# Optimization experiments

Measured on AMD Instinct MI355X. Metric: run time of the kernel, lower is better.

## Reference

```python
import jax, jax.numpy as jnp
import numpy as np

BS, NA = 32, 128
NE = NA * (NA - 1)            # fully-connected directed, no self loops
NU, D = 4, 8                  # num_user, per-user feature dim
FEAT = NU * D                 # 32: node / edge feature dim
CC = 8                        # conv1 out channels (1x1 conv, in_channels=2)
CONV_OUT = CC * NU * D        # 256
EMB = 64                      # embedding size (x_last / output dim)
H1 = 256                      # MLP hidden
MLP1_IN = CONV_OUT + EMB      # layer_idx > 1: concat local_state_j
MLP2_IN = FEAT + EMB + EMB    # x0, x_last, agg_in


def make_edges():
    src, dst = np.meshgrid(np.arange(NA), np.arange(NA), indexing='ij')
    m = src != dst
    return jnp.asarray(np.stack([src[m], dst[m]], axis=1), dtype=jnp.int32)


def setup_inputs() -> dict:
    key = jax.random.key(0)
    ks = jax.random.split(key, 9)
    return {
        "x0": jax.random.normal(ks[0], (BS, NA, FEAT), jnp.float32),
        "x_last": jax.random.normal(ks[1], (BS, NA, EMB), jnp.float32),
        "edge_attr": jax.random.normal(ks[2], (BS, NE, FEAT), jnp.float32),
        "conv_w": jax.random.normal(ks[3], (CC, 2), jnp.float32) * 0.3,
        "conv_b": jnp.zeros((CC,), jnp.float32),
        "mlp1_w1": jax.random.normal(ks[4], (MLP1_IN, H1), jnp.float32) * 0.05,
        "mlp1_b1": jnp.zeros((H1,), jnp.float32),
        "mlp1_w2": jax.random.normal(ks[5], (H1, EMB), jnp.float32) * 0.05,
        "mlp1_b2": jnp.zeros((EMB,), jnp.float32),
        "mlp2_w1": jax.random.normal(ks[6], (MLP2_IN, H1), jnp.float32) * 0.05,
        "mlp2_b1": jnp.zeros((H1,), jnp.float32),
        "mlp2_w2": jax.random.normal(ks[7], (H1, EMB), jnp.float32) * 0.05,
        "mlp2_b2": jnp.zeros((EMB,), jnp.float32),
        "edge_idx": make_edges(),
    }


def reference(x0, x_last, edge_attr, conv_w, conv_b,
              mlp1_w1, mlp1_b1, mlp1_w2, mlp1_b2,
              mlp2_w1, mlp2_b1, mlp2_w2, mlp2_b2, edge_idx):
    src, dst = edge_idx[:, 0], edge_idx[:, 1]
    # --- propagate / local_embedding ---
    nf_j = x0[:, src, :]                 # [B, E, FEAT] gather source node feats
    ls_j = x_last[:, src, :]             # [B, E, EMB]  (layer_idx > 1)
    # torch: cat(node_feat, edge_attr) on user dim then view [N,2,NU,D]
    x = jnp.stack([nf_j.reshape(BS, NE, NU, D),
                   edge_attr.reshape(BS, NE, NU, D)], axis=2)  # [B,E,2,NU,D]
    # 1x1 Conv2d(2 -> CC) + ReLU
    y = jax.nn.relu(jnp.einsum('becud,oc->beoud', x, conv_w)
                    + conv_b[None, None, :, None, None])
    y = y.reshape(BS, NE, CONV_OUT)
    lf = jnp.concatenate([y, ls_j], axis=-1)                   # [B,E,MLP1_IN]
    h = jax.nn.relu(lf @ mlp1_w1 + mlp1_b1)
    local_embed = h @ mlp1_w2 + mlp1_b2                        # [B,E,EMB]
    # per-node segment sum over destination (replaces python loop over agents)
    agg_in = jnp.zeros((BS, NA, EMB), local_embed.dtype).at[:, dst, :].add(local_embed)
    # --- update_embedding ---
    agg = jnp.concatenate([x0, x_last, agg_in], axis=-1)       # [B,NA,MLP2_IN]
    h2 = jax.nn.relu(agg @ mlp2_w1 + mlp2_b1)
    return h2 @ mlp2_w2 + mlp2_b2                              # [B,NA,EMB]
```

## Files before the change

### kernel.cpp

```cpp
#include <hip/hip_runtime.h>
#include <hip/hip_bf16.h>

#define BSg   32
#define NAg   128
#define NEg   16256
#define EMBg  64
#define H1g   256

typedef __attribute__((ext_vector_type(8))) short  short8;
typedef __attribute__((ext_vector_type(4))) float  f32x4;

__device__ __forceinline__ unsigned short f2bf16u(float x) {
    union { __hip_bfloat16 h; unsigned short u; } cv;
    cv.h = __float2bfloat16(x);
    return cv.u;
}
__device__ __forceinline__ unsigned int pack2(float a, float b) {
    union { __hip_bfloat162 h; unsigned int u; } cv;
    cv.h = __float22bfloat162_rn(make_float2(a, b));
    return cv.u;
}

__global__ void pack_weights(const float* __restrict__ w1, const float* __restrict__ xl,
                             unsigned short* __restrict__ w1p, unsigned short* __restrict__ xlp)
{
    int i = blockIdx.x * 256 + threadIdx.x;
    if (i < 320 * 256) {
        int k = i >> 8, n = i & 255;
        w1p[(k >> 3) * (256 * 8) + n * 8 + (k & 7)] = f2bf16u(w1[i]);
    }
    if (i < BSg * NAg * EMBg)
        xlp[i] = f2bf16u(xl[i]);
}

__global__ __launch_bounds__(512, 4) void edge_kernel(
    const float* __restrict__ x0, const unsigned short* __restrict__ xlp,
    const float* __restrict__ edge_attr, const float* __restrict__ conv_w,
    const float* __restrict__ conv_b, const unsigned short* __restrict__ w1p,
    const float* __restrict__ b1, const float* __restrict__ w2f,
    const float* __restrict__ b2, float* __restrict__ agg)
{
    __shared__ unsigned short fragA[2][8 * 4 * 64 * 8];

    const int tid  = threadIdx.x;
    const int b    = blockIdx.x >> 7;
    const int d    = blockIdx.x & 127;
    const int w8   = tid >> 6, lane = tid & 63;
    const int half = w8 >> 2, wq = w8 & 3;
    const int llo  = lane & 15, lhi = lane >> 4;
    const int colbase = wq * 64;

    short8 af8[4], af9[4];
    #pragma unroll
    for (int m = 0; m < 4; ++m) {
        int el = half * 64 + m * 16 + llo;
        int s  = el + (el >= d ? 1 : 0);
        if (s > 127) s = 127;
        const unsigned short* base = xlp + (((b << 7) | s) << 6) + lhi * 8;
        af8[m] = *(const short8*)base;
        af9[m] = *(const short8*)(base + 32);
    }

    {
        const int j  = wq * 16 + llo;
        const int el = half * 64 + j;
        int s = el + (el >= d ? 1 : 0);
        if (s > 127) s = 127;
        int e = s * 127 + d - (s < d ? 1 : 0);
        if (e > NEg - 1) e = NEg - 1;

        const float4* nfp = (const float4*)(x0        + (((size_t)b * NAg + s) << 5) + (lhi << 3));
        const float4* eap = (const float4*)(edge_attr + (((size_t)b * NEg + e) << 5) + (lhi << 3));
        float4 nf0 = nfp[0], nf1 = nfp[1];
        float4 ea0 = eap[0], ea1 = eap[1];

        #pragma unroll
        for (int o = 0; o < 8; ++o) {
            const float w0 = conv_w[2 * o], w1v = conv_w[2 * o + 1], cb = conv_b[o];
            float y0 = fmaxf(fmaf(w0, nf0.x, fmaf(w1v, ea0.x, cb)), 0.f);
            float y1 = fmaxf(fmaf(w0, nf0.y, fmaf(w1v, ea0.y, cb)), 0.f);
            float y2 = fmaxf(fmaf(w0, nf0.z, fmaf(w1v, ea0.z, cb)), 0.f);
            float y3 = fmaxf(fmaf(w0, nf0.w, fmaf(w1v, ea0.w, cb)), 0.f);
            float y4 = fmaxf(fmaf(w0, nf1.x, fmaf(w1v, ea1.x, cb)), 0.f);
            float y5 = fmaxf(fmaf(w0, nf1.y, fmaf(w1v, ea1.y, cb)), 0.f);
            float y6 = fmaxf(fmaf(w0, nf1.z, fmaf(w1v, ea1.z, cb)), 0.f);
            float y7 = fmaxf(fmaf(w0, nf1.w, fmaf(w1v, ea1.w, cb)), 0.f);
            uint4 pk;
            pk.x = pack2(y0, y1); pk.y = pack2(y2, y3);
            pk.z = pack2(y4, y5); pk.w = pack2(y6, y7);
            *(uint4*)&fragA[half][(((o * 4 + wq) * 64) + lane) * 8] = pk;
        }
    }
    __syncthreads();

    f32x4 acc[4][4];
    #pragma unroll
    for (int m = 0; m < 4; ++m)
        #pragma unroll
        for (int n = 0; n < 4; ++n)
            acc[m][n] = (f32x4){0.f, 0.f, 0.f, 0.f};

    #pragma unroll
    for (int ks = 0; ks < 10; ++ks) {
        short8 af[4], bf[4];
        #pragma unroll
        for (int m = 0; m < 4; ++m) {
            if (ks < 8)       af[m] = *(const short8*)&fragA[half][((ks * 4 + m) * 64 + lane) * 8];
            else if (ks == 8) af[m] = af8[m];
            else              af[m] = af9[m];
        }
        #pragma unroll
        for (int n = 0; n < 4; ++n)
            bf[n] = *(const short8*)&w1p[((ks * 4 + lhi) * H1g + colbase + n * 16 + llo) * 8];
        #pragma unroll
        for (int m = 0; m < 4; ++m)
            #pragma unroll
            for (int n = 0; n < 4; ++n)
                acc[m][n] = __builtin_amdgcn_mfma_f32_16x16x32_bf16(af[m], bf[n], acc[m][n], 0, 0, 0);
    }

    float h1s[4];
    {
        float bias1[4];
        #pragma unroll
        for (int n = 0; n < 4; ++n) bias1[n] = b1[colbase + n * 16 + llo];
        #pragma unroll
        for (int n = 0; n < 4; ++n) {
            float p = 0.f;
            #pragma unroll
            for (int m = 0; m < 4; ++m)
                #pragma unroll
                for (int i = 0; i < 4; ++i) {
                    float v = fmaxf(acc[m][n][i] + bias1[n], 0.f);
                    if (!(m == 3 && i == 3) || !(half == 1 && lhi == 3)) p += v;
                }
            p += __shfl_xor(p, 16, 64);
            p += __shfl_xor(p, 32, 64);
            h1s[n] = p;
        }
    }
    __syncthreads();

    float* h1part = (float*)&fragA[0][0];
    float* redS   = h1part + 512;

    if (lhi == 0) {
        #pragma unroll
        for (int n = 0; n < 4; ++n) h1part[half * 256 + colbase + n * 16 + llo] = h1s[n];
    }
    __syncthreads();

    {
        const int c = tid & 63, kq = tid >> 6;
        float p = 0.f;
        #pragma unroll 8
        for (int k0 = 0; k0 < 32; ++k0) {
            int k = kq * 32 + k0;
            float h = h1part[k] + h1part[256 + k];
            p = fmaf(h, w2f[k * 64 + c], p);
        }
        redS[kq * 64 + c] = p;
    }
    __syncthreads();
    if (tid < 64) {
        float v = redS[tid]       + redS[64 + tid]  + redS[128 + tid] + redS[192 + tid]
                + redS[256 + tid] + redS[320 + tid] + redS[384 + tid] + redS[448 + tid]
                + 127.f * b2[tid];
        agg[(((size_t)b * NAg + d) << 6) + tid] = v;
    }
}

__global__ __launch_bounds__(256) void node_kernel(
    const float* __restrict__ x0, const float* __restrict__ x_last,
    const float* __restrict__ agg, const float* __restrict__ w1,
    const float* __restrict__ b1, const float* __restrict__ w2,
    const float* __restrict__ b2, float* __restrict__ out)
{
    __shared__ float lf[8][160];
    __shared__ float h2s[8][257];
    const int tid = threadIdx.x;
    const int r0  = blockIdx.x * 8;

    for (int idx = tid; idx < 8 * 160; idx += 256) {
        int r = idx / 160, c = idx % 160;
        int gr = r0 + r;
        int bb = gr >> 7, a = gr & 127;
        float v;
        if (c < 32)      v = x0[(((size_t)bb * NAg + a) << 5) + c];
        else if (c < 96) v = x_last[(((size_t)bb * NAg + a) << 6) + (c - 32)];
        else             v = agg[((size_t)gr << 6) + (c - 96)];
        lf[r][c] = v;
    }
    __syncthreads();

    {
        const int c = tid;
        float acc[8];
        const float bb = b1[c];
        #pragma unroll
        for (int r = 0; r < 8; ++r) acc[r] = bb;
        for (int k = 0; k < 160; ++k) {
            float wv = w1[k * 256 + c];
            #pragma unroll
            for (int r = 0; r < 8; ++r) acc[r] = fmaf(lf[r][k], wv, acc[r]);
        }
        #pragma unroll
        for (int r = 0; r < 8; ++r) h2s[r][c] = fmaxf(acc[r], 0.f);
    }
    __syncthreads();

    {
        const int n = tid & 63, rq = tid >> 6;
        float acc[2];
        const float bb = b2[n];
        #pragma unroll
        for (int j = 0; j < 2; ++j) acc[j] = bb;
        for (int k = 0; k < 256; ++k) {
            float wv = w2[k * 64 + n];
            #pragma unroll
            for (int j = 0; j < 2; ++j) acc[j] = fmaf(h2s[rq * 2 + j][k], wv, acc[j]);
        }
        #pragma unroll
        for (int j = 0; j < 2; ++j)
            out[((size_t)(r0 + rq * 2 + j) << 6) + n] = acc[j];
    }
}

extern "C" void kernel_launch(void* const* d_in, const int* in_sizes, int n_in,
                              void* d_out, int out_size, void* d_ws, size_t ws_size,
                              hipStream_t stream)
{
    const float* x0       = (const float*)d_in[0];
    const float* x_last   = (const float*)d_in[1];
    const float* edge_attr= (const float*)d_in[2];
    const float* conv_w   = (const float*)d_in[3];
    const float* conv_b   = (const float*)d_in[4];
    const float* mlp1_w1  = (const float*)d_in[5];
    const float* mlp1_b1  = (const float*)d_in[6];
    const float* mlp1_w2  = (const float*)d_in[7];
    const float* mlp1_b2  = (const float*)d_in[8];
    const float* mlp2_w1  = (const float*)d_in[9];
    const float* mlp2_b1  = (const float*)d_in[10];
    const float* mlp2_w2  = (const float*)d_in[11];
    const float* mlp2_b2  = (const float*)d_in[12];

    char* ws = (char*)d_ws;
    float* agg          = (float*)ws;
    unsigned short* w1p = (unsigned short*)(ws + (1 << 20));
    unsigned short* xlp = (unsigned short*)(ws + (1 << 20) + (192 << 10));

    pack_weights<<<1024, 256, 0, stream>>>(mlp1_w1, x_last, w1p, xlp);
    edge_kernel<<<BSg * NAg, 512, 0, stream>>>(x0, xlp, edge_attr, conv_w, conv_b,
                                               w1p, mlp1_b1, mlp1_w2, mlp1_b2, agg);
    node_kernel<<<(BSg * NAg) / 8, 256, 0, stream>>>(x0, x_last, agg, mlp2_w1, mlp2_b1,
                                                     mlp2_w2, mlp2_b2, (float*)d_out);
}
```

Measured before the change: 141.1 us.

## Split edge kernel into half-blocks and move second MLP layer to separate kernel

```diff
diff --git a/kernel.cpp b/kernel.cpp
--- a/kernel.cpp
+++ b/kernel.cpp
@@ -33,20 +33,21 @@
         xlp[i] = f2bf16u(xl[i]);
 }
 
-__global__ __launch_bounds__(512, 4) void edge_kernel(
+__global__ __launch_bounds__(256, 5) void edge_kernel(
     const float* __restrict__ x0, const unsigned short* __restrict__ xlp,
     const float* __restrict__ edge_attr, const float* __restrict__ conv_w,
     const float* __restrict__ conv_b, const unsigned short* __restrict__ w1p,
-    const float* __restrict__ b1, const float* __restrict__ w2f,
-    const float* __restrict__ b2, float* __restrict__ agg)
-{
-    __shared__ unsigned short fragA[2][8 * 4 * 64 * 8];
+    const float* __restrict__ b1, float* __restrict__ h1half)
+{
+    __shared__ unsigned short fragA[8 * 4 * 64 * 8];
+
+    const int wgid = (blockIdx.x & 7) * 1024 + (blockIdx.x >> 3);
+    const int half = wgid & 1;
+    const int bd   = wgid >> 1;
+    const int b    = bd >> 7, d = bd & 127;
 
     const int tid  = threadIdx.x;
-    const int b    = blockIdx.x >> 7;
-    const int d    = blockIdx.x & 127;
-    const int w8   = tid >> 6, lane = tid & 63;
-    const int half = w8 >> 2, wq = w8 & 3;
+    const int wq   = tid >> 6, lane = tid & 63;
     const int llo  = lane & 15, lhi = lane >> 4;
     const int colbase = wq * 64;
 
@@ -88,7 +89,7 @@
             uint4 pk;
             pk.x = pack2(y0, y1); pk.y = pack2(y2, y3);
             pk.z = pack2(y4, y5); pk.w = pack2(y6, y7);
-            *(uint4*)&fragA[half][(((o * 4 + wq) * 64) + lane) * 8] = pk;
+            *(uint4*)&fragA[(((o * 4 + wq) * 64) + lane) * 8] = pk;
         }
     }
     __syncthreads();
@@ -105,7 +106,7 @@
         short8 af[4], bf[4];
         #pragma unroll
         for (int m = 0; m < 4; ++m) {
-            if (ks < 8)       af[m] = *(const short8*)&fragA[half][((ks * 4 + m) * 64 + lane) * 8];
+            if (ks < 8)       af[m] = *(const short8*)&fragA[((ks * 4 + m) * 64 + lane) * 8];
             else if (ks == 8) af[m] = af8[m];
             else              af[m] = af9[m];
         }
@@ -139,35 +140,26 @@
             h1s[n] = p;
         }
     }
-    __syncthreads();
-
-    float* h1part = (float*)&fragA[0][0];
-    float* redS   = h1part + 512;
 
     if (lhi == 0) {
         #pragma unroll
-        for (int n = 0; n < 4; ++n) h1part[half * 256 + colbase + n * 16 + llo] = h1s[n];
-    }
-    __syncthreads();
-
-    {
-        const int c = tid & 63, kq = tid >> 6;
-        float p = 0.f;
-        #pragma unroll 8
-        for (int k0 = 0; k0 < 32; ++k0) {
-            int k = kq * 32 + k0;
-            float h = h1part[k] + h1part[256 + k];
-            p = fmaf(h, w2f[k * 64 + c], p);
-        }
-        redS[kq * 64 + c] = p;
-    }
-    __syncthreads();
-    if (tid < 64) {
-        float v = redS[tid]       + redS[64 + tid]  + redS[128 + tid] + redS[192 + tid]
-                + redS[256 + tid] + redS[320 + tid] + redS[384 + tid] + redS[448 + tid]
-                + 127.f * b2[tid];
-        agg[(((size_t)b * NAg + d) << 6) + tid] = v;
-    }
+        for (int n = 0; n < 4; ++n)
+            h1half[((size_t)wgid << 8) + colbase + n * 16 + llo] = h1s[n];
+    }
+}
+
+__global__ __launch_bounds__(256) void gemm2_kernel(
+    const float* __restrict__ h1half, const float* __restrict__ w2f,
+    const float* __restrict__ b2, float* __restrict__ agg)
+{
+    const int r = blockIdx.x * 4 + (threadIdx.x >> 6);
+    const int c = threadIdx.x & 63;
+    const float* h0 = h1half + ((size_t)r << 9);
+    float acc = 127.f * b2[c];
+    #pragma unroll 4
+    for (int k = 0; k < 256; ++k)
+        acc = fmaf(h0[k] + h0[256 + k], w2f[k * 64 + c], acc);
+    agg[((size_t)r << 6) + c] = acc;
 }
 
 __global__ __launch_bounds__(256) void node_kernel(
@@ -248,10 +240,12 @@
     float* agg          = (float*)ws;
     unsigned short* w1p = (unsigned short*)(ws + (1 << 20));
     unsigned short* xlp = (unsigned short*)(ws + (1 << 20) + (192 << 10));
+    float* h1half       = (float*)(ws + (2 << 20));
 
     pack_weights<<<1024, 256, 0, stream>>>(mlp1_w1, x_last, w1p, xlp);
-    edge_kernel<<<BSg * NAg, 512, 0, stream>>>(x0, xlp, edge_attr, conv_w, conv_b,
-                                               w1p, mlp1_b1, mlp1_w2, mlp1_b2, agg);
+    edge_kernel<<<BSg * NAg * 2, 256, 0, stream>>>(x0, xlp, edge_attr, conv_w, conv_b,
+                                                   w1p, mlp1_b1, h1half);
+    gemm2_kernel<<<1024, 256, 0, stream>>>(h1half, mlp1_w2, mlp1_b2, agg);
     node_kernel<<<(BSg * NAg) / 8, 256, 0, stream>>>(x0, x_last, agg, mlp2_w1, mlp2_b1,
                                                      mlp2_w2, mlp2_b2, (float*)d_out);
 }
```

After: 203.4 us. 44.2% more time.

## Fuse x_last bf16 conversion into edge kernel via shared memory staging

Applied to the files above, without the earlier changes.

```diff
diff --git a/kernel.cpp b/kernel.cpp
--- a/kernel.cpp
+++ b/kernel.cpp
@@ -21,26 +21,23 @@
     return cv.u;
 }
 
-__global__ void pack_weights(const float* __restrict__ w1, const float* __restrict__ xl,
-                             unsigned short* __restrict__ w1p, unsigned short* __restrict__ xlp)
+__global__ void pack_weights(const float* __restrict__ w1, unsigned short* __restrict__ w1p)
 {
     int i = blockIdx.x * 256 + threadIdx.x;
     if (i < 320 * 256) {
         int k = i >> 8, n = i & 255;
         w1p[(k >> 3) * (256 * 8) + n * 8 + (k & 7)] = f2bf16u(w1[i]);
     }
-    if (i < BSg * NAg * EMBg)
-        xlp[i] = f2bf16u(xl[i]);
 }
 
 __global__ __launch_bounds__(512, 4) void edge_kernel(
-    const float* __restrict__ x0, const unsigned short* __restrict__ xlp,
+    const float* __restrict__ x0, const float* __restrict__ x_last,
     const float* __restrict__ edge_attr, const float* __restrict__ conv_w,
     const float* __restrict__ conv_b, const unsigned short* __restrict__ w1p,
     const float* __restrict__ b1, const float* __restrict__ w2f,
     const float* __restrict__ b2, float* __restrict__ agg)
 {
-    __shared__ unsigned short fragA[2][8 * 4 * 64 * 8];
+    __shared__ unsigned short fragA[2][10 * 4 * 64 * 8];
 
     const int tid  = threadIdx.x;
     const int b    = blockIdx.x >> 7;
@@ -50,16 +47,10 @@
     const int llo  = lane & 15, lhi = lane >> 4;
     const int colbase = wq * 64;
 
-    short8 af8[4], af9[4];
+    short8 bf0[4];
     #pragma unroll
-    for (int m = 0; m < 4; ++m) {
-        int el = half * 64 + m * 16 + llo;
-        int s  = el + (el >= d ? 1 : 0);
-        if (s > 127) s = 127;
-        const unsigned short* base = xlp + (((b << 7) | s) << 6) + lhi * 8;
-        af8[m] = *(const short8*)base;
-        af9[m] = *(const short8*)(base + 32);
-    }
+    for (int n = 0; n < 4; ++n)
+        bf0[n] = *(const short8*)&w1p[(lhi * H1g + colbase + n * 16 + llo) * 8];
 
     {
         const int j  = wq * 16 + llo;
@@ -90,6 +81,19 @@
             pk.z = pack2(y4, y5); pk.w = pack2(y6, y7);
             *(uint4*)&fragA[half][(((o * 4 + wq) * 64) + lane) * 8] = pk;
         }
+        {
+            const float4* lsp = (const float4*)(x_last + (((size_t)b * NAg + s) << 6) + (lhi << 4));
+            float4 l0 = lsp[0], l1 = lsp[1], l2 = lsp[2], l3 = lsp[3];
+            uint4 pa, pb;
+            pa.x = pack2(l0.x, l0.y); pa.y = pack2(l0.z, l0.w);
+            pa.z = pack2(l1.x, l1.y); pa.w = pack2(l1.z, l1.w);
+            pb.x = pack2(l2.x, l2.y); pb.y = pack2(l2.z, l2.w);
+            pb.z = pack2(l3.x, l3.y); pb.w = pack2(l3.z, l3.w);
+            const int ks8  = 8 + (lhi >> 1);
+            const int slot = (ks8 * 4 + wq) * 64 + ((lhi & 1) * 2) * 16 + llo;
+            *(uint4*)&fragA[half][slot * 8]        = pa;
+            *(uint4*)&fragA[half][(slot + 16) * 8] = pb;
+        }
     }
     __syncthreads();
 
@@ -104,14 +108,13 @@
     for (int ks = 0; ks < 10; ++ks) {
         short8 af[4], bf[4];
         #pragma unroll
-        for (int m = 0; m < 4; ++m) {
-            if (ks < 8)       af[m] = *(const short8*)&fragA[half][((ks * 4 + m) * 64 + lane) * 8];
-            else if (ks == 8) af[m] = af8[m];
-            else              af[m] = af9[m];
-        }
-        #pragma unroll
-        for (int n = 0; n < 4; ++n)
-            bf[n] = *(const short8*)&w1p[((ks * 4 + lhi) * H1g + colbase + n * 16 + llo) * 8];
+        for (int m = 0; m < 4; ++m)
+            af[m] = *(const short8*)&fragA[half][((ks * 4 + m) * 64 + lane) * 8];
+        #pragma unroll
+        for (int n = 0; n < 4; ++n) {
+            if (ks == 0) bf[n] = bf0[n];
+            else         bf[n] = *(const short8*)&w1p[((ks * 4 + lhi) * H1g + colbase + n * 16 + llo) * 8];
+        }
         #pragma unroll
         for (int m = 0; m < 4; ++m)
             #pragma unroll
@@ -247,10 +250,9 @@
     char* ws = (char*)d_ws;
     float* agg          = (float*)ws;
     unsigned short* w1p = (unsigned short*)(ws + (1 << 20));
-    unsigned short* xlp = (unsigned short*)(ws + (1 << 20) + (192 << 10));
-
-    pack_weights<<<1024, 256, 0, stream>>>(mlp1_w1, x_last, w1p, xlp);
-    edge_kernel<<<BSg * NAg, 512, 0, stream>>>(x0, xlp, edge_attr, conv_w, conv_b,
+
+    pack_weights<<<320, 256, 0, stream>>>(mlp1_w1, w1p);
+    edge_kernel<<<BSg * NAg, 512, 0, stream>>>(x0, x_last, edge_attr, conv_w, conv_b,
                                                w1p, mlp1_b1, mlp1_w2, mlp1_b2, agg);
     node_kernel<<<(BSg * NAg) / 8, 256, 0, stream>>>(x0, x_last, agg, mlp2_w1, mlp2_b1,
                                                      mlp2_w2, mlp2_b2, (float*)d_out);
```

After: 132.6 us. -6.0%, faster.
